# Performance work log

Hardware: AMD Instinct MI355X
Metric: run time of the kernel (lower is better)

The kernel has to match this reference:

```python
import jax, jax.numpy as jnp
import numpy as np

N, S, F, E, H, O, L, FE = 8, 1024, 64, 512, 8, 64, 6, 4
HD = E // H
FF = FE * E


def setup_inputs() -> dict:
    key = jax.random.key(0)
    ks = iter(jax.random.split(key, 40))
    def rn(shape, s=0.02):
        return jax.random.normal(next(ks), shape, jnp.float32) * s
    return {
        'x': jax.random.normal(next(ks), (N, F, S), jnp.float32),
        'W_first': rn((F, E)), 'b_first': jnp.zeros((E,), jnp.float32),
        'pos_emb': rn((S, E)),
        'Wq': rn((L, HD, HD)), 'bq': jnp.zeros((L, HD), jnp.float32),
        'Wk': rn((L, HD, HD)), 'bk': jnp.zeros((L, HD), jnp.float32),
        'Wv': rn((L, HD, HD)), 'bv': jnp.zeros((L, HD), jnp.float32),
        'Wo': rn((L, E, E)), 'bo': jnp.zeros((L, E), jnp.float32),
        'g1': jnp.ones((L, E), jnp.float32), 'be1': jnp.zeros((L, E), jnp.float32),
        'Wf1': rn((L, E, FF)), 'bf1': jnp.zeros((L, FF), jnp.float32),
        'Wf2': rn((L, FF, E)), 'bf2': jnp.zeros((L, E), jnp.float32),
        'g2': jnp.ones((L, E), jnp.float32), 'be2': jnp.zeros((L, E), jnp.float32),
        'Wfin': rn((E, O)), 'bfin': jnp.zeros((O,), jnp.float32),
    }


def layernorm(x, g, b, eps=1e-5):
    m = jnp.mean(x, axis=-1, keepdims=True)
    v = jnp.mean(jnp.square(x - m), axis=-1, keepdims=True)
    return (x - m) * jax.lax.rsqrt(v + eps) * g + b


def reference(x, W_first, b_first, pos_emb, Wq, bq, Wk, bk, Wv, bv, Wo, bo,
              g1, be1, Wf1, bf1, Wf2, bf2, g2, be2, Wfin, bfin):
    # x: (N, F, S) -> (N, S, F)
    h = jax.nn.relu(jnp.einsum('nfs,fe->nse', x, W_first) + b_first) + pos_emb[None]
    scale = E ** 0.5  # note: module scales by sqrt(embed_size), not sqrt(head_dim)
    for i in range(L):
        t = h.reshape(N, S, H, HD)
        q = jnp.einsum('nshd,de->nshe', t, Wq[i]) + bq[i]
        k = jnp.einsum('nshd,de->nshe', t, Wk[i]) + bk[i]
        v = jnp.einsum('nshd,de->nshe', t, Wv[i]) + bv[i]
        energy = jnp.einsum('nqhd,nkhd->nhqk', q, k)  # (N,H,S,S)
        att = jax.nn.softmax(energy / scale, axis=-1)
        o = jnp.einsum('nhqk,nkhd->nqhd', att, v).reshape(N, S, E)
        o = jnp.einsum('nse,ef->nsf', o, Wo[i]) + bo[i]
        hx = layernorm(o + h, g1[i], be1[i])
        ff = jax.nn.relu(jnp.einsum('nse,ef->nsf', hx, Wf1[i]) + bf1[i])
        ff = jnp.einsum('nsf,fe->nse', ff, Wf2[i]) + bf2[i]
        h = layernorm(ff + hx, g2[i], be2[i])
    # Conv1d kernel_size=1 == pointwise linear over channels; output (N, O, S)
    return jnp.einsum('nse,eo->nos', h, Wfin) + bfin[None, :, None]
```

## Files before the change

### kernel.cpp

```cpp
#include <hip/hip_runtime.h>
#include <hip/hip_bf16.h>
#include <math.h>

#define N_ 8
#define S_ 1024
#define F_ 64
#define E_ 512
#define H_ 8
#define O_ 64
#define L_ 6
#define HD_ 64
#define FF_ 2048
#define SCALE_ 0.044194173824159216f
#define LOG2E_ 1.4426950408889634f
#define QSCALE_ (SCALE_ * LOG2E_)

typedef unsigned short u16;
typedef __attribute__((ext_vector_type(4))) unsigned short u16x4;
typedef __attribute__((ext_vector_type(8))) unsigned short u16x8;
typedef __attribute__((ext_vector_type(8))) short short8;
typedef __attribute__((ext_vector_type(4))) float floatx4;

__device__ __forceinline__ u16 f2b(float f) {
    union { float f; unsigned u; } v; v.f = f;
    unsigned u = v.u;
    unsigned r = (u + 0x7FFFu + ((u >> 16) & 1u)) >> 16;
    return (u16)r;
}
__device__ __forceinline__ u16 f2b_fast(float f) {
    union { float f; unsigned u; } v; v.f = f;
    return (u16)((v.u + 0x8000u) >> 16);
}
__device__ __forceinline__ float b2f(u16 h) {
    union { unsigned u; float f; } v; v.u = ((unsigned)h) << 16;
    return v.f;
}

__device__ __forceinline__ void gload16(const u16* g, u16* l) {
    __builtin_amdgcn_global_load_lds(
        (const __attribute__((address_space(1))) void*)g,
        (__attribute__((address_space(3))) void*)l, 16, 0, 0);
}

__global__ __launch_bounds__(256) void first_mfma(
    const float* __restrict__ x, const u16* __restrict__ wt,
    const float* __restrict__ bf, const float* __restrict__ pe,
    u16* __restrict__ resb)
{
    __shared__ u16 a_s[128][72];
    int t = threadIdx.x;
    int w = t >> 6, lane = t & 63, quad = lane >> 4, c16 = lane & 15;
    int rowhalf = w >> 1, colhalf = w & 1;
    int col0 = blockIdx.x * 128;
    int row0 = blockIdx.y * 128;
    int n = row0 >> 10, s0 = row0 & 1023;

    const float* xb = x + (size_t)n * F_ * S_ + s0;
    #pragma unroll
    for (int i = 0; i < 8; i++) {
        int pos = (t + i * 256) * 4;
        int f = pos >> 7, sl = pos & 127;
        float4 v = *(const float4*)&xb[(size_t)f * S_ + sl];
        a_s[sl + 0][f] = f2b_fast(v.x);
        a_s[sl + 1][f] = f2b_fast(v.y);
        a_s[sl + 2][f] = f2b_fast(v.z);
        a_s[sl + 3][f] = f2b_fast(v.w);
    }
    __syncthreads();

    floatx4 acc[4][4];
    #pragma unroll
    for (int mt = 0; mt < 4; mt++)
        #pragma unroll
        for (int nt = 0; nt < 4; nt++) acc[mt][nt] = (floatx4){0.f, 0.f, 0.f, 0.f};

    #pragma unroll
    for (int ks = 0; ks < 2; ks++) {
        short8 af[4], bfr[4];
        #pragma unroll
        for (int mt = 0; mt < 4; mt++)
            af[mt] = *(const short8*)&a_s[rowhalf * 64 + mt * 16 + c16][ks * 32 + quad * 8];
        #pragma unroll
        for (int nt = 0; nt < 4; nt++)
            bfr[nt] = *(const short8*)&wt[(size_t)(col0 + colhalf * 64 + nt * 16 + c16) * F_
                                          + ks * 32 + quad * 8];
        #pragma unroll
        for (int mt = 0; mt < 4; mt++)
            #pragma unroll
            for (int nt = 0; nt < 4; nt++)
                acc[mt][nt] = __builtin_amdgcn_mfma_f32_16x16x32_bf16(
                    af[mt], bfr[nt], acc[mt][nt], 0, 0, 0);
    }

    #pragma unroll
    for (int nt = 0; nt < 4; nt++) {
        int col = col0 + colhalf * 64 + nt * 16 + c16;
        float bv = bf[col];
        #pragma unroll
        for (int mt = 0; mt < 4; mt++) {
            #pragma unroll
            for (int r = 0; r < 4; r++) {
                size_t row = (size_t)row0 + rowhalf * 64 + mt * 16 + quad * 4 + r;
                int s = (int)(row & 1023);
                float v = fmaxf(acc[mt][nt][r] + bv, 0.f) + pe[(size_t)s * E_ + col];
                resb[row * E_ + col] = f2b_fast(v);
            }
        }
    }
}

__global__ __launch_bounds__(256) void wcast_t(
    const float* __restrict__ W0, u16* __restrict__ Wt0, int K, int Nc)
{
    __shared__ float tile[32][33];
    int t = threadIdx.x;
    int bx = blockIdx.x, by = blockIdx.y;
    const float* W = W0 + (size_t)blockIdx.z * K * Nc;
    u16* Wt = Wt0 + (size_t)blockIdx.z * K * Nc;
    #pragma unroll
    for (int i = 0; i < 4; i++) {
        int q = t + i * 256; int r = q >> 5, c = q & 31;
        tile[r][c] = W[(size_t)(by * 32 + r) * Nc + bx * 32 + c];
    }
    __syncthreads();
    #pragma unroll
    for (int i = 0; i < 4; i++) {
        int q = t + i * 256; int r = q >> 5, c = q & 31;
        Wt[(size_t)(bx * 32 + r) * K + by * 32 + c] = f2b(tile[c][r]);
    }
}

__global__ __launch_bounds__(256) void qkvw_cast(
    const float* __restrict__ Wq, const float* __restrict__ Wk,
    const float* __restrict__ Wv,
    u16* __restrict__ wqt, u16* __restrict__ wkt, u16* __restrict__ wvt)
{
    int l = blockIdx.x;
    int t = threadIdx.x;
    size_t off = (size_t)l * HD_ * HD_;
    #pragma unroll
    for (int i = 0; i < 16; i++) {
        int idx = t + i * 256;
        int e = idx >> 6, d = idx & 63;
        wqt[off + idx] = f2b(Wq[off + d * HD_ + e]);
        wkt[off + idx] = f2b(Wk[off + d * HD_ + e]);
        wvt[off + idx] = f2b(Wv[off + d * HD_ + e]);
    }
}

__global__ __launch_bounds__(256) void qkv_mfma(
    const u16* __restrict__ hb,
    const u16* __restrict__ wqt, const u16* __restrict__ wkt,
    const u16* __restrict__ wvt,
    const float* __restrict__ bq, const float* __restrict__ bk,
    const float* __restrict__ bv,
    u16* __restrict__ qo, u16* __restrict__ ko, u16* __restrict__ vo)
{
    __shared__ u16 a_s[256][72];
    int t = threadIdx.x;
    int w = t >> 6, lane = t & 63, quad = lane >> 4, c16 = lane & 15;
    size_t row0 = (size_t)blockIdx.x * 256;

    #pragma unroll
    for (int i = 0; i < 8; i++) {
        int q = t + i * 256; int r = q >> 3, c = q & 7;
        *(u16x8*)&a_s[r][c * 8] = *(const u16x8*)&hb[(row0 + r) * HD_ + c * 8];
    }
    __syncthreads();

    short8 af[4][2];
    #pragma unroll
    for (int mt = 0; mt < 4; mt++)
        #pragma unroll
        for (int ks = 0; ks < 2; ks++)
            af[mt][ks] = *(const short8*)&a_s[w * 64 + mt * 16 + c16][ks * 32 + quad * 8];

    const u16* wts[3] = {wqt, wkt, wvt};
    const float* bs[3] = {bq, bk, bv};
    u16* outs[3] = {qo, ko, vo};

    #pragma unroll
    for (int m = 0; m < 3; m++) {
        short8 bfr[4][2];
        #pragma unroll
        for (int nt = 0; nt < 4; nt++)
            #pragma unroll
            for (int ks = 0; ks < 2; ks++)
                bfr[nt][ks] = *(const short8*)&wts[m][(nt * 16 + c16) * HD_ + ks * 32 + quad * 8];
        floatx4 acc[4][4];
        #pragma unroll
        for (int mt = 0; mt < 4; mt++)
            #pragma unroll
            for (int nt = 0; nt < 4; nt++) acc[mt][nt] = (floatx4){0.f, 0.f, 0.f, 0.f};
        #pragma unroll
        for (int ks = 0; ks < 2; ks++)
            #pragma unroll
            for (int mt = 0; mt < 4; mt++)
                #pragma unroll
                for (int nt = 0; nt < 4; nt++)
                    acc[mt][nt] = __builtin_amdgcn_mfma_f32_16x16x32_bf16(
                        af[mt][ks], bfr[nt][ks], acc[mt][nt], 0, 0, 0);
        float osc = (m == 0) ? QSCALE_ : 1.0f;
        #pragma unroll
        for (int nt = 0; nt < 4; nt++) {
            float bv_ = bs[m][nt * 16 + c16];
            #pragma unroll
            for (int mt = 0; mt < 4; mt++)
                #pragma unroll
                for (int r = 0; r < 4; r++)
                    outs[m][(row0 + w * 64 + mt * 16 + quad * 4 + r) * HD_ + nt * 16 + c16] =
                        f2b_fast((acc[mt][nt][r] + bv_) * osc);
        }
    }
}

__global__ __launch_bounds__(256) void vtrans(
    const u16* __restrict__ vb, u16* __restrict__ vt)
{
    int bid = blockIdx.x;
    int st = bid & 15, hh = (bid >> 4) & 7, n = bid >> 7;
    __shared__ u16 tile[64][72];
    int t = threadIdx.x;
    #pragma unroll
    for (int i = 0; i < 2; i++) {
        int q = t + i * 256; int sl = q >> 3, c = q & 7;
        *(u16x8*)&tile[sl][c * 8] =
            *(const u16x8*)&vb[(((size_t)(n * S_ + st * 64 + sl)) * H_ + hh) * 64 + c * 8];
    }
    __syncthreads();
    #pragma unroll
    for (int i = 0; i < 2; i++) {
        int q = t + i * 256; int d = q >> 3, sc = q & 7;
        u16x8 v;
        #pragma unroll
        for (int j = 0; j < 8; j++) v[j] = tile[sc * 8 + j][d];
        *(u16x8*)&vt[((size_t)(n * H_ + hh) * 64 + d) * (size_t)S_ + st * 64 + sc * 8] = v;
    }
}

__global__ __launch_bounds__(256, 2) void attn_mfma(
    const u16* __restrict__ Q, const u16* __restrict__ K,
    const u16* __restrict__ Vt, u16* __restrict__ O)
{
    int bid = blockIdx.x;
    int qt = bid & 7, hh = (bid >> 3) & 7, n = bid >> 6;
    int t = threadIdx.x;
    int w = t >> 6, lane = t & 63, quad = lane >> 4, c16 = lane & 15;

    __shared__ u16 qp_s[128][72];
    __shared__ u16 k_s[64][72];
    __shared__ u16 vt_s[64][72];
    u16 (*p_s)[72] = &qp_s[w * 32];

    const size_t qkbase = (size_t)n * S_ * E_ + hh * 64;
    const size_t vtbase = ((size_t)(n * H_ + hh) * 64) * (size_t)S_;

    #pragma unroll
    for (int i = 0; i < 4; i++) {
        int q = t + i * 256; int r = q >> 3, c = q & 7;
        *(u16x8*)&qp_s[r][c * 8] =
            *(const u16x8*)&Q[qkbase + (size_t)(qt * 128 + r) * E_ + c * 8];
    }
    __syncthreads();

    short8 qf[2][2];
    #pragma unroll
    for (int nq = 0; nq < 2; nq++)
        #pragma unroll
        for (int ks = 0; ks < 2; ks++)
            qf[nq][ks] = *(const short8*)&qp_s[w * 32 + nq * 16 + c16][ks * 32 + quad * 8];

    const short8 ones = {(short)0x3F80, (short)0x3F80, (short)0x3F80, (short)0x3F80,
                         (short)0x3F80, (short)0x3F80, (short)0x3F80, (short)0x3F80};

    floatx4 oaccT[4][2];
    floatx4 lacc[2];
    #pragma unroll
    for (int nq = 0; nq < 2; nq++) {
        lacc[nq] = (floatx4){0.f, 0.f, 0.f, 0.f};
        #pragma unroll
        for (int mt = 0; mt < 4; mt++) oaccT[mt][nq] = (floatx4){0.f, 0.f, 0.f, 0.f};
    }

    int ar = t >> 3, acq = (t & 7) * 8;
    u16x8 pk[2], pv[2];
    #pragma unroll
    for (int i = 0; i < 2; i++) {
        pk[i] = *(const u16x8*)&K[qkbase + (size_t)(ar + i * 32) * E_ + acq];
        pv[i] = *(const u16x8*)&Vt[vtbase + (size_t)(ar + i * 32) * S_ + acq];
    }

    for (int k0 = 0; k0 < S_; k0 += 64) {
        #pragma unroll
        for (int i = 0; i < 2; i++) {
            *(u16x8*)&k_s[ar + i * 32][acq] = pk[i];
            *(u16x8*)&vt_s[ar + i * 32][acq] = pv[i];
        }
        __syncthreads();
        if (k0 + 64 < S_) {
            #pragma unroll
            for (int i = 0; i < 2; i++) {
                pk[i] = *(const u16x8*)&K[qkbase + (size_t)(k0 + 64 + ar + i * 32) * E_ + acq];
                pv[i] = *(const u16x8*)&Vt[vtbase + (size_t)(ar + i * 32) * S_ + k0 + 64 + acq];
            }
        }

        floatx4 st[4][2];
        #pragma unroll
        for (int mt = 0; mt < 4; mt++)
            #pragma unroll
            for (int nq = 0; nq < 2; nq++) st[mt][nq] = (floatx4){0.f, 0.f, 0.f, 0.f};
        #pragma unroll
        for (int ks = 0; ks < 2; ks++) {
            short8 kf[4];
            #pragma unroll
            for (int mt = 0; mt < 4; mt++)
                kf[mt] = *(const short8*)&k_s[mt * 16 + c16][ks * 32 + quad * 8];
            #pragma unroll
            for (int mt = 0; mt < 4; mt++)
                #pragma unroll
                for (int nq = 0; nq < 2; nq++)
                    st[mt][nq] = __builtin_amdgcn_mfma_f32_16x16x32_bf16(
                        kf[mt], qf[nq][ks], st[mt][nq], 0, 0, 0);
        }

        #pragma unroll
        for (int nq = 0; nq < 2; nq++)
            #pragma unroll
            for (int mt = 0; mt < 4; mt++) {
                u16x4 h;
                #pragma unroll
                for (int r = 0; r < 4; r++) h[r] = f2b_fast(exp2f(st[mt][nq][r]));
                *(u16x4*)&p_s[nq * 16 + c16][mt * 16 + quad * 4] = h;
            }

        #pragma unroll
        for (int ks = 0; ks < 2; ks++) {
            short8 pf[2];
            #pragma unroll
            for (int nq = 0; nq < 2; nq++)
                pf[nq] = *(const short8*)&p_s[nq * 16 + c16][ks * 32 + quad * 8];
            short8 vf[4];
            #pragma unroll
            for (int mt = 0; mt < 4; mt++)
                vf[mt] = *(const short8*)&vt_s[mt * 16 + c16][ks * 32 + quad * 8];
            #pragma unroll
            for (int nq = 0; nq < 2; nq++) {
                lacc[nq] = __builtin_amdgcn_mfma_f32_16x16x32_bf16(ones, pf[nq], lacc[nq], 0, 0, 0);
                #pragma unroll
                for (int mt = 0; mt < 4; mt++)
                    oaccT[mt][nq] = __builtin_amdgcn_mfma_f32_16x16x32_bf16(
                        vf[mt], pf[nq], oaccT[mt][nq], 0, 0, 0);
            }
        }
        __syncthreads();
    }

    #pragma unroll
    for (int nq = 0; nq < 2; nq++) {
        float rl = 1.f / lacc[nq][0];
        int s = qt * 128 + w * 32 + nq * 16 + c16;
        size_t base = (size_t)(n * S_ + s) * E_ + hh * 64;
        #pragma unroll
        for (int mt = 0; mt < 4; mt++) {
            u16x4 h;
            #pragma unroll
            for (int r = 0; r < 4; r++) h[r] = f2b_fast(oaccT[mt][nq][r] * rl);
            *(u16x4*)&O[base + mt * 16 + quad * 4] = h;
        }
    }
}

template <int MT, int NT, bool RELU, bool HASRES, bool OUTF32, bool OUTBF16>
__global__ __launch_bounds__(256, 2) void gemm_mfma(
    const u16* __restrict__ A, const u16* __restrict__ Bt,
    const float* __restrict__ bias, const u16* __restrict__ resid,
    float* __restrict__ outf, u16* __restrict__ outb, int M, int Nc, int K)
{
    constexpr int MFR = MT / 32;
    constexpr int NFR = NT / 32;
    constexpr int AI  = MT / 32;
    constexpr int BI  = NT / 32;
    __shared__ u16 a_s[MT * 64];
    __shared__ u16 b_s[NT * 64];

    int t = threadIdx.x;
    int w = t >> 6, lane = t & 63, quad = lane >> 4, c16 = lane & 15;
    int rw = w >> 1, cw = w & 1;

    int gx = gridDim.x;
    int nwg = gx * (int)gridDim.y;
    int lin = (int)blockIdx.y * gx + (int)blockIdx.x;
    int cpx = nwg >> 3;
    int id2 = (lin & 7) * cpx + (lin >> 3);
    int bx = id2 % gx, by = id2 / gx;

    size_t row0 = (size_t)by * MT;
    size_t col0 = (size_t)bx * NT;

    size_t aoff[AI]; int adst[AI];
    #pragma unroll
    for (int i = 0; i < AI; i++) {
        int p = t + i * 256;
        int r = p >> 3;
        int kch = (p & 7) ^ (r & 7);
        aoff[i] = (row0 + r) * (size_t)K + kch * 8;
        adst[i] = w * 512 + i * 2048;
    }
    size_t boff[BI]; int bdst[BI];
    #pragma unroll
    for (int i = 0; i < BI; i++) {
        int p = t + i * 256;
        int r = p >> 3;
        int kch = (p & 7) ^ (r & 7);
        boff[i] = (col0 + r) * (size_t)K + kch * 8;
        bdst[i] = w * 512 + i * 2048;
    }

    floatx4 acc[MFR][NFR];
    #pragma unroll
    for (int mt = 0; mt < MFR; mt++)
        #pragma unroll
        for (int nt = 0; nt < NFR; nt++) acc[mt][nt] = (floatx4){0.f, 0.f, 0.f, 0.f};

    for (int k0 = 0; k0 < K; k0 += 64) {
        #pragma unroll
        for (int i = 0; i < AI; i++) gload16(A + aoff[i] + k0, a_s + adst[i]);
        #pragma unroll
        for (int i = 0; i < BI; i++) gload16(Bt + boff[i] + k0, b_s + bdst[i]);
        __syncthreads();

        #pragma unroll
        for (int ks = 0; ks < 2; ks++) {
            short8 af[MFR], bfr[NFR];
            #pragma unroll
            for (int mt = 0; mt < MFR; mt++) {
                int r = rw * (MT / 2) + mt * 16 + c16;
                af[mt] = *(const short8*)&a_s[r * 64 + (((ks * 4 + quad) ^ (r & 7)) * 8)];
            }
            #pragma unroll
            for (int nt = 0; nt < NFR; nt++) {
                int r = cw * (NT / 2) + nt * 16 + c16;
                bfr[nt] = *(const short8*)&b_s[r * 64 + (((ks * 4 + quad) ^ (r & 7)) * 8)];
            }
            #pragma unroll
            for (int mt = 0; mt < MFR; mt++)
                #pragma unroll
                for (int nt = 0; nt < NFR; nt++)
                    acc[mt][nt] = __builtin_amdgcn_mfma_f32_16x16x32_bf16(
                        af[mt], bfr[nt], acc[mt][nt], 0, 0, 0);
        }
        __syncthreads();
    }

    #pragma unroll
    for (int nt = 0; nt < NFR; nt++) {
        int col = (int)col0 + cw * (NT / 2) + nt * 16 + c16;
        float bv = bias[col];
        #pragma unroll
        for (int mt = 0; mt < MFR; mt++) {
            size_t rowb = row0 + rw * (MT / 2) + mt * 16 + quad * 4;
            #pragma unroll
            for (int r = 0; r < 4; r++) {
                size_t row = rowb + r;
                float v = acc[mt][nt][r] + bv;
                if constexpr (HASRES) v += b2f(resid[row * Nc + col]);
                if constexpr (RELU) v = fmaxf(v, 0.f);
                if constexpr (OUTF32) outf[row * Nc + col] = v;
                if constexpr (OUTBF16) outb[row * Nc + col] = f2b_fast(v);
            }
        }
    }
}

__global__ __launch_bounds__(256) void layernorm_k(
    const float* __restrict__ in, const float* __restrict__ g,
    const float* __restrict__ bb, u16* __restrict__ outb)
{
    int row = blockIdx.x;
    int t = threadIdx.x;
    const float* x = in + (size_t)row * E_;
    float x0 = x[t], x1 = x[t + 256];
    float s = x0 + x1;
    #pragma unroll
    for (int off = 32; off; off >>= 1) s += __shfl_down(s, off, 64);
    __shared__ float red[4];
    int wid = t >> 6, lane = t & 63;
    if (lane == 0) red[wid] = s;
    __syncthreads();
    float m = (red[0] + red[1] + red[2] + red[3]) * (1.f / E_);
    float d0 = x0 - m, d1 = x1 - m;
    float sq = d0 * d0 + d1 * d1;
    #pragma unroll
    for (int off = 32; off; off >>= 1) sq += __shfl_down(sq, off, 64);
    __syncthreads();
    if (lane == 0) red[wid] = sq;
    __syncthreads();
    float var = (red[0] + red[1] + red[2] + red[3]) * (1.f / E_);
    float rstd = rsqrtf(var + 1e-5f);
    outb[(size_t)row * E_ + t] = f2b_fast(d0 * rstd * g[t] + bb[t]);
    outb[(size_t)row * E_ + t + 256] = f2b_fast(d1 * rstd * g[t + 256] + bb[t + 256]);
}

__global__ __launch_bounds__(256) void final_mfma(
    const u16* __restrict__ hb, const u16* __restrict__ wft,
    const float* __restrict__ bfin, float* __restrict__ outp)
{
    __shared__ u16 a_s[64][72];
    int t = threadIdx.x;
    int w = t >> 6, lane = t & 63, quad = lane >> 4, c16 = lane & 15;
    size_t row0 = (size_t)blockIdx.x * 64;

    floatx4 acc[4];
    #pragma unroll
    for (int nt = 0; nt < 4; nt++) acc[nt] = (floatx4){0.f, 0.f, 0.f, 0.f};

    int ar = t >> 3, acq = (t & 7) * 8;
    u16x8 pa[2];
    #pragma unroll
    for (int i = 0; i < 2; i++)
        pa[i] = *(const u16x8*)&hb[(row0 + ar + i * 32) * E_ + acq];

    for (int k0 = 0; k0 < E_; k0 += 64) {
        #pragma unroll
        for (int i = 0; i < 2; i++)
            *(u16x8*)&a_s[ar + i * 32][acq] = pa[i];
        __syncthreads();
        if (k0 + 64 < E_) {
            #pragma unroll
            for (int i = 0; i < 2; i++)
                pa[i] = *(const u16x8*)&hb[(row0 + ar + i * 32) * E_ + k0 + 64 + acq];
        }
        #pragma unroll
        for (int ks = 0; ks < 2; ks++) {
            short8 af = *(const short8*)&a_s[w * 16 + c16][ks * 32 + quad * 8];
            #pragma unroll
            for (int nt = 0; nt < 4; nt++) {
                short8 bf = *(const short8*)&wft[(nt * 16 + c16) * E_ + k0 + ks * 32 + quad * 8];
                acc[nt] = __builtin_amdgcn_mfma_f32_16x16x32_bf16(af, bf, acc[nt], 0, 0, 0);
            }
        }
        __syncthreads();
    }

    #pragma unroll
    for (int nt = 0; nt < 4; nt++) {
        int o = nt * 16 + c16;
        float bv = bfin[o];
        #pragma unroll
        for (int r = 0; r < 4; r++) {
            size_t row = row0 + w * 16 + quad * 4 + r;
            int n = (int)(row >> 10), s = (int)(row & 1023);
            outp[((size_t)(n * O_ + o)) * S_ + s] = acc[nt][r] + bv;
        }
    }
}

extern "C" void kernel_launch(void* const* d_in, const int* in_sizes, int n_in,
                              void* d_out, int out_size, void* d_ws, size_t ws_size,
                              hipStream_t stream)
{
    const float* x       = (const float*)d_in[0];
    const float* W_first = (const float*)d_in[1];
    const float* b_first = (const float*)d_in[2];
    const float* pos_emb = (const float*)d_in[3];
    const float* Wq      = (const float*)d_in[4];
    const float* bq      = (const float*)d_in[5];
    const float* Wk      = (const float*)d_in[6];
    const float* bk      = (const float*)d_in[7];
    const float* Wv      = (const float*)d_in[8];
    const float* bv      = (const float*)d_in[9];
    const float* Wo      = (const float*)d_in[10];
    const float* bo      = (const float*)d_in[11];
    const float* g1      = (const float*)d_in[12];
    const float* be1     = (const float*)d_in[13];
    const float* Wf1     = (const float*)d_in[14];
    const float* bf1     = (const float*)d_in[15];
    const float* Wf2     = (const float*)d_in[16];
    const float* bf2     = (const float*)d_in[17];
    const float* g2      = (const float*)d_in[18];
    const float* be2     = (const float*)d_in[19];
    const float* Wfin    = (const float*)d_in[20];
    const float* bfin    = (const float*)d_in[21];
    float* out = (float*)d_out;

    const size_t M4 = (size_t)N_ * S_ * E_;
    float* t1   = (float*)d_ws;
    u16*   resb = (u16*)(t1 + M4);
    u16*   qb   = resb + M4;
    u16*   kb   = qb + M4;
    u16*   vb   = kb + M4;
    u16*   vt   = vb + M4;
    u16*   ob   = vt + M4;
    u16*   ffb  = qb;
    u16*   wot  = ob + M4;
    u16*   wf1t = wot + (size_t)L_ * E_ * E_;
    u16*   wf2t = wf1t + (size_t)L_ * E_ * FF_;
    u16*   wqt  = wf2t + (size_t)L_ * FF_ * E_;
    u16*   wkt  = wqt + (size_t)L_ * HD_ * HD_;
    u16*   wvt  = wkt + (size_t)L_ * HD_ * HD_;
    u16*   wft  = wvt + (size_t)L_ * HD_ * HD_;
    u16*   w1t  = wft + (size_t)O_ * E_;

    const int rows = N_ * S_;

    qkvw_cast<<<L_, 256, 0, stream>>>(Wq, Wk, Wv, wqt, wkt, wvt);
    wcast_t<<<dim3(E_ / 32, F_ / 32, 1), 256, 0, stream>>>(W_first, w1t, F_, E_);
    wcast_t<<<dim3(E_ / 32, E_ / 32, L_), 256, 0, stream>>>(Wo, wot, E_, E_);
    wcast_t<<<dim3(FF_ / 32, E_ / 32, L_), 256, 0, stream>>>(Wf1, wf1t, E_, FF_);
    wcast_t<<<dim3(E_ / 32, FF_ / 32, L_), 256, 0, stream>>>(Wf2, wf2t, FF_, E_);
    wcast_t<<<dim3(O_ / 32, E_ / 32, 1), 256, 0, stream>>>(Wfin, wft, E_, O_);

    first_mfma<<<dim3(E_ / 128, rows / 128), 256, 0, stream>>>(
        x, w1t, b_first, pos_emb, resb);

    for (int i = 0; i < L_; i++) {
        qkv_mfma<<<256, 256, 0, stream>>>(
            resb, wqt + (size_t)i * HD_ * HD_, wkt + (size_t)i * HD_ * HD_,
            wvt + (size_t)i * HD_ * HD_, bq + i * HD_, bk + i * HD_, bv + i * HD_,
            qb, kb, vb);
        vtrans<<<1024, 256, 0, stream>>>(vb, vt);
        attn_mfma<<<512, 256, 0, stream>>>(qb, kb, vt, ob);
        gemm_mfma<128, 64, false, true, true, false><<<dim3(E_ / 64, rows / 128), 256, 0, stream>>>(
            ob, wot + (size_t)i * E_ * E_, bo + i * E_, resb, t1, nullptr, rows, E_, E_);
        layernorm_k<<<rows, 256, 0, stream>>>(t1, g1 + i * E_, be1 + i * E_, resb);
        gemm_mfma<128, 128, true, false, false, true><<<dim3(FF_ / 128, rows / 128), 256, 0, stream>>>(
            resb, wf1t + (size_t)i * E_ * FF_, bf1 + i * FF_, nullptr, nullptr, ffb,
            rows, FF_, E_);
        gemm_mfma<128, 64, false, true, true, false><<<dim3(E_ / 64, rows / 128), 256, 0, stream>>>(
            ffb, wf2t + (size_t)i * FF_ * E_, bf2 + i * E_, resb, t1, nullptr,
            rows, E_, FF_);
        layernorm_k<<<rows, 256, 0, stream>>>(t1, g2 + i * E_, be2 + i * E_, resb);
    }

    final_mfma<<<rows / 64, 256, 0, stream>>>(resb, wft, bfin, out);
}
```

Baseline: 1.037 ms.

## Halve attention and QKV tiles, XOR-swizzle shared memory, remap blocks, add setprio

The attention kernel now handles 64 queries per block instead of 128, which doubles the grid and raises the launch-bounds occupancy hint to 4 blocks per CU. Blocks are remapped so that neighbouring block IDs work on different (n, head) pairs. All shared tiles drop row padding in favour of an XOR swizzle to avoid bank conflicts, and s_setprio brackets the MFMA phases. The QKV and vtrans kernels get the same swizzle, and QKV tiles shrink to 128 rows. The intent is more parallelism and latency hiding. The cost is that K/V tiles are reloaded twice as often per query, which raises global and L2 traffic.

```diff
diff --git a/kernel.cpp b/kernel.cpp
--- a/kernel.cpp
+++ b/kernel.cpp
@@ -156,24 +156,27 @@
     const float* __restrict__ bv,
     u16* __restrict__ qo, u16* __restrict__ ko, u16* __restrict__ vo)
 {
-    __shared__ u16 a_s[256][72];
+    __shared__ u16 a_s[128 * 64];
     int t = threadIdx.x;
     int w = t >> 6, lane = t & 63, quad = lane >> 4, c16 = lane & 15;
-    size_t row0 = (size_t)blockIdx.x * 256;
-
-    #pragma unroll
-    for (int i = 0; i < 8; i++) {
+    size_t row0 = (size_t)blockIdx.x * 128;
+
+    #pragma unroll
+    for (int i = 0; i < 4; i++) {
         int q = t + i * 256; int r = q >> 3, c = q & 7;
-        *(u16x8*)&a_s[r][c * 8] = *(const u16x8*)&hb[(row0 + r) * HD_ + c * 8];
-    }
-    __syncthreads();
-
-    short8 af[4][2];
-    #pragma unroll
-    for (int mt = 0; mt < 4; mt++)
-        #pragma unroll
-        for (int ks = 0; ks < 2; ks++)
-            af[mt][ks] = *(const short8*)&a_s[w * 64 + mt * 16 + c16][ks * 32 + quad * 8];
+        *(u16x8*)&a_s[r * 64 + ((c ^ (r & 7)) * 8)] =
+            *(const u16x8*)&hb[(row0 + r) * HD_ + c * 8];
+    }
+    __syncthreads();
+
+    short8 af[2][2];
+    #pragma unroll
+    for (int mt = 0; mt < 2; mt++)
+        #pragma unroll
+        for (int ks = 0; ks < 2; ks++) {
+            int r = w * 32 + mt * 16 + c16;
+            af[mt][ks] = *(const short8*)&a_s[r * 64 + (((ks * 4 + quad) ^ (r & 7)) * 8)];
+        }
 
     const u16* wts[3] = {wqt, wkt, wvt};
     const float* bs[3] = {bq, bk, bv};
@@ -187,15 +190,15 @@
             #pragma unroll
             for (int ks = 0; ks < 2; ks++)
                 bfr[nt][ks] = *(const short8*)&wts[m][(nt * 16 + c16) * HD_ + ks * 32 + quad * 8];
-        floatx4 acc[4][4];
-        #pragma unroll
-        for (int mt = 0; mt < 4; mt++)
+        floatx4 acc[2][4];
+        #pragma unroll
+        for (int mt = 0; mt < 2; mt++)
             #pragma unroll
             for (int nt = 0; nt < 4; nt++) acc[mt][nt] = (floatx4){0.f, 0.f, 0.f, 0.f};
         #pragma unroll
         for (int ks = 0; ks < 2; ks++)
             #pragma unroll
-            for (int mt = 0; mt < 4; mt++)
+            for (int mt = 0; mt < 2; mt++)
                 #pragma unroll
                 for (int nt = 0; nt < 4; nt++)
                     acc[mt][nt] = __builtin_amdgcn_mfma_f32_16x16x32_bf16(
@@ -205,10 +208,10 @@
         for (int nt = 0; nt < 4; nt++) {
             float bv_ = bs[m][nt * 16 + c16];
             #pragma unroll
-            for (int mt = 0; mt < 4; mt++)
+            for (int mt = 0; mt < 2; mt++)
                 #pragma unroll
                 for (int r = 0; r < 4; r++)
-                    outs[m][(row0 + w * 64 + mt * 16 + quad * 4 + r) * HD_ + nt * 16 + c16] =
+                    outs[m][(row0 + w * 32 + mt * 16 + quad * 4 + r) * HD_ + nt * 16 + c16] =
                         f2b_fast((acc[mt][nt][r] + bv_) * osc);
         }
     }
@@ -219,12 +222,12 @@
 {
     int bid = blockIdx.x;
     int st = bid & 15, hh = (bid >> 4) & 7, n = bid >> 7;
-    __shared__ u16 tile[64][72];
+    __shared__ u16 tile[64 * 64];
     int t = threadIdx.x;
     #pragma unroll
     for (int i = 0; i < 2; i++) {
         int q = t + i * 256; int sl = q >> 3, c = q & 7;
-        *(u16x8*)&tile[sl][c * 8] =
+        *(u16x8*)&tile[sl * 64 + ((c ^ ((sl >> 3) & 7)) * 8)] =
             *(const u16x8*)&vb[(((size_t)(n * S_ + st * 64 + sl)) * H_ + hh) * 64 + c * 8];
     }
     __syncthreads();
@@ -233,56 +236,57 @@
         int q = t + i * 256; int d = q >> 3, sc = q & 7;
         u16x8 v;
         #pragma unroll
-        for (int j = 0; j < 8; j++) v[j] = tile[sc * 8 + j][d];
+        for (int j = 0; j < 8; j++) {
+            int row = sc * 8 + j;
+            v[j] = tile[row * 64 + (((d >> 3) ^ (row >> 3)) * 8) + (d & 7)];
+        }
         *(u16x8*)&vt[((size_t)(n * H_ + hh) * 64 + d) * (size_t)S_ + st * 64 + sc * 8] = v;
     }
 }
 
-__global__ __launch_bounds__(256, 2) void attn_mfma(
+__global__ __launch_bounds__(256, 4) void attn_mfma(
     const u16* __restrict__ Q, const u16* __restrict__ K,
     const u16* __restrict__ Vt, u16* __restrict__ O)
 {
-    int bid = blockIdx.x;
-    int qt = bid & 7, hh = (bid >> 3) & 7, n = bid >> 6;
+    int bid0 = blockIdx.x;
+    int bid = (bid0 & 7) * 128 + (bid0 >> 3);
+    int qt = bid & 15, hh = (bid >> 4) & 7, n = bid >> 7;
     int t = threadIdx.x;
     int w = t >> 6, lane = t & 63, quad = lane >> 4, c16 = lane & 15;
 
-    __shared__ u16 qp_s[128][72];
-    __shared__ u16 k_s[64][72];
-    __shared__ u16 vt_s[64][72];
-    u16 (*p_s)[72] = &qp_s[w * 32];
+    __shared__ u16 qp_s[64 * 64];
+    __shared__ u16 k_s[64 * 64];
+    __shared__ u16 vt_s[64 * 64];
+    u16* p_s = qp_s + w * 16 * 64;
 
     const size_t qkbase = (size_t)n * S_ * E_ + hh * 64;
     const size_t vtbase = ((size_t)(n * H_ + hh) * 64) * (size_t)S_;
 
     #pragma unroll
-    for (int i = 0; i < 4; i++) {
+    for (int i = 0; i < 2; i++) {
         int q = t + i * 256; int r = q >> 3, c = q & 7;
-        *(u16x8*)&qp_s[r][c * 8] =
-            *(const u16x8*)&Q[qkbase + (size_t)(qt * 128 + r) * E_ + c * 8];
-    }
-    __syncthreads();
-
-    short8 qf[2][2];
-    #pragma unroll
-    for (int nq = 0; nq < 2; nq++)
-        #pragma unroll
-        for (int ks = 0; ks < 2; ks++)
-            qf[nq][ks] = *(const short8*)&qp_s[w * 32 + nq * 16 + c16][ks * 32 + quad * 8];
+        *(u16x8*)&qp_s[r * 64 + ((c ^ (r & 7)) * 8)] =
+            *(const u16x8*)&Q[qkbase + (size_t)(qt * 64 + r) * E_ + c * 8];
+    }
+    __syncthreads();
+
+    short8 qf[2];
+    #pragma unroll
+    for (int ks = 0; ks < 2; ks++) {
+        int r = w * 16 + c16;
+        qf[ks] = *(const short8*)&qp_s[r * 64 + (((ks * 4 + quad) ^ (r & 7)) * 8)];
+    }
 
     const short8 ones = {(short)0x3F80, (short)0x3F80, (short)0x3F80, (short)0x3F80,
                          (short)0x3F80, (short)0x3F80, (short)0x3F80, (short)0x3F80};
 
-    floatx4 oaccT[4][2];
-    floatx4 lacc[2];
-    #pragma unroll
-    for (int nq = 0; nq < 2; nq++) {
-        lacc[nq] = (floatx4){0.f, 0.f, 0.f, 0.f};
-        #pragma unroll
-        for (int mt = 0; mt < 4; mt++) oaccT[mt][nq] = (floatx4){0.f, 0.f, 0.f, 0.f};
-    }
-
-    int ar = t >> 3, acq = (t & 7) * 8;
+    floatx4 oaccT[4];
+    floatx4 lacc = (floatx4){0.f, 0.f, 0.f, 0.f};
+    #pragma unroll
+    for (int mt = 0; mt < 4; mt++) oaccT[mt] = (floatx4){0.f, 0.f, 0.f, 0.f};
+
+    int ar = t >> 3, act = t & 7;
+    int acq = act * 8;
     u16x8 pk[2], pv[2];
     #pragma unroll
     for (int i = 0; i < 2; i++) {
@@ -293,8 +297,10 @@
     for (int k0 = 0; k0 < S_; k0 += 64) {
         #pragma unroll
         for (int i = 0; i < 2; i++) {
-            *(u16x8*)&k_s[ar + i * 32][acq] = pk[i];
-            *(u16x8*)&vt_s[ar + i * 32][acq] = pv[i];
+            int r = ar + i * 32;
+            int sc = (act ^ (r & 7)) * 8;
+            *(u16x8*)&k_s[r * 64 + sc] = pk[i];
+            *(u16x8*)&vt_s[r * 64 + sc] = pv[i];
         }
         __syncthreads();
         if (k0 + 64 < S_) {
@@ -305,67 +311,63 @@
             }
         }
 
-        floatx4 st[4][2];
-        #pragma unroll
-        for (int mt = 0; mt < 4; mt++)
-            #pragma unroll
-            for (int nq = 0; nq < 2; nq++) st[mt][nq] = (floatx4){0.f, 0.f, 0.f, 0.f};
+        floatx4 st[4];
+        #pragma unroll
+        for (int mt = 0; mt < 4; mt++) st[mt] = (floatx4){0.f, 0.f, 0.f, 0.f};
+        __builtin_amdgcn_s_setprio(1);
         #pragma unroll
         for (int ks = 0; ks < 2; ks++) {
             short8 kf[4];
             #pragma unroll
+            for (int mt = 0; mt < 4; mt++) {
+                int r = mt * 16 + c16;
+                kf[mt] = *(const short8*)&k_s[r * 64 + (((ks * 4 + quad) ^ (r & 7)) * 8)];
+            }
+            #pragma unroll
             for (int mt = 0; mt < 4; mt++)
-                kf[mt] = *(const short8*)&k_s[mt * 16 + c16][ks * 32 + quad * 8];
-            #pragma unroll
-            for (int mt = 0; mt < 4; mt++)
-                #pragma unroll
-                for (int nq = 0; nq < 2; nq++)
-                    st[mt][nq] = __builtin_amdgcn_mfma_f32_16x16x32_bf16(
-                        kf[mt], qf[nq][ks], st[mt][nq], 0, 0, 0);
-        }
-
-        #pragma unroll
-        for (int nq = 0; nq < 2; nq++)
-            #pragma unroll
-            for (int mt = 0; mt < 4; mt++) {
-                u16x4 h;
-                #pragma unroll
-                for (int r = 0; r < 4; r++) h[r] = f2b_fast(exp2f(st[mt][nq][r]));
-                *(u16x4*)&p_s[nq * 16 + c16][mt * 16 + quad * 4] = h;
-            }
-
-        #pragma unroll
-        for (int ks = 0; ks < 2; ks++) {
-            short8 pf[2];
-            #pragma unroll
-            for (int nq = 0; nq < 2; nq++)
-                pf[nq] = *(const short8*)&p_s[nq * 16 + c16][ks * 32 + quad * 8];
-            short8 vf[4];
-            #pragma unroll
-            for (int mt = 0; mt < 4; mt++)
-                vf[mt] = *(const short8*)&vt_s[mt * 16 + c16][ks * 32 + quad * 8];
-            #pragma unroll
-            for (int nq = 0; nq < 2; nq++) {
-                lacc[nq] = __builtin_amdgcn_mfma_f32_16x16x32_bf16(ones, pf[nq], lacc[nq], 0, 0, 0);
-                #pragma unroll
-                for (int mt = 0; mt < 4; mt++)
-                    oaccT[mt][nq] = __builtin_amdgcn_mfma_f32_16x16x32_bf16(
-                        vf[mt], pf[nq], oaccT[mt][nq], 0, 0, 0);
-            }
-        }
-        __syncthreads();
-    }
-
-    #pragma unroll
-    for (int nq = 0; nq < 2; nq++) {
-        float rl = 1.f / lacc[nq][0];
-        int s = qt * 128 + w * 32 + nq * 16 + c16;
-        size_t base = (size_t)(n * S_ + s) * E_ + hh * 64;
+                st[mt] = __builtin_amdgcn_mfma_f32_16x16x32_bf16(
+                    kf[mt], qf[ks], st[mt], 0, 0, 0);
+        }
+        __builtin_amdgcn_s_setprio(0);
+
         #pragma unroll
         for (int mt = 0; mt < 4; mt++) {
             u16x4 h;
             #pragma unroll
-            for (int r = 0; r < 4; r++) h[r] = f2b_fast(oaccT[mt][nq][r] * rl);
+            for (int r = 0; r < 4; r++) h[r] = f2b_fast(exp2f(st[mt][r]));
+            *(u16x4*)&p_s[c16 * 64 + (((2 * mt + (quad >> 1)) ^ (c16 & 7)) * 8)
+                          + (quad & 1) * 4] = h;
+        }
+
+        __builtin_amdgcn_s_setprio(1);
+        #pragma unroll
+        for (int ks = 0; ks < 2; ks++) {
+            short8 pf = *(const short8*)&p_s[c16 * 64 + (((ks * 4 + quad) ^ (c16 & 7)) * 8)];
+            short8 vf[4];
+            #pragma unroll
+            for (int mt = 0; mt < 4; mt++) {
+                int r = mt * 16 + c16;
+                vf[mt] = *(const short8*)&vt_s[r * 64 + (((ks * 4 + quad) ^ (r & 7)) * 8)];
+            }
+            lacc = __builtin_amdgcn_mfma_f32_16x16x32_bf16(ones, pf, lacc, 0, 0, 0);
+            #pragma unroll
+            for (int mt = 0; mt < 4; mt++)
+                oaccT[mt] = __builtin_amdgcn_mfma_f32_16x16x32_bf16(
+                    vf[mt], pf, oaccT[mt], 0, 0, 0);
+        }
+        __builtin_amdgcn_s_setprio(0);
+        __syncthreads();
+    }
+
+    {
+        float rl = 1.f / lacc[0];
+        int s = qt * 64 + w * 16 + c16;
+        size_t base = (size_t)(n * S_ + s) * E_ + hh * 64;
+        #pragma unroll
+        for (int mt = 0; mt < 4; mt++) {
+            u16x4 h;
+            #pragma unroll
+            for (int r = 0; r < 4; r++) h[r] = f2b_fast(oaccT[mt][r] * rl);
             *(u16x4*)&O[base + mt * 16 + quad * 4] = h;
         }
     }
@@ -615,12 +617,12 @@
         x, w1t, b_first, pos_emb, resb);
 
     for (int i = 0; i < L_; i++) {
-        qkv_mfma<<<256, 256, 0, stream>>>(
+        qkv_mfma<<<512, 256, 0, stream>>>(
             resb, wqt + (size_t)i * HD_ * HD_, wkt + (size_t)i * HD_ * HD_,
             wvt + (size_t)i * HD_ * HD_, bq + i * HD_, bk + i * HD_, bv + i * HD_,
             qb, kb, vb);
         vtrans<<<1024, 256, 0, stream>>>(vb, vt);
-        attn_mfma<<<512, 256, 0, stream>>>(qb, kb, vt, ob);
+        attn_mfma<<<1024, 256, 0, stream>>>(qb, kb, vt, ob);
         gemm_mfma<128, 64, false, true, true, false><<<dim3(E_ / 64, rows / 128), 256, 0, stream>>>(
             ob, wot + (size_t)i * E_ * E_, bo + i * E_, resb, t1, nullptr, rows, E_, E_);
         layernorm_k<<<rows, 256, 0, stream>>>(t1, g1 + i * E_, be1 + i * E_, resb);
```

New measurement: 1.026 ms. About the same (-1.0%).
